# Performance work log

Measured on AMD Instinct MI355X. Metric: run time of the kernel, lower is better.

The kernel has to match this reference:

```python
import jax, jax.numpy as jnp
from jax import lax
import numpy as np

RATIO = 0.25
RADIUS = 0.2


def _fps(xyz, npoint):
    # iterative farthest point sampling, sequential over npoint via lax.scan
    B, N, _ = xyz.shape
    far0 = jax.random.randint(jax.random.key(42), (B,), 0, N)
    dist0 = jnp.full((B, N), 1e10, xyz.dtype)

    def step(carry, _):
        distance, far = carry
        centroid = jnp.take_along_axis(xyz, far[:, None, None], axis=1)  # (B,1,3)
        d = jnp.sum((xyz - centroid) ** 2, axis=-1)                      # (B,N)
        distance = jnp.minimum(distance, d)
        return (distance, jnp.argmax(distance, axis=-1)), far

    _, idxs = lax.scan(step, (dist0, far0), None, length=npoint)  # (npoint,B)
    return jnp.transpose(idxs)  # (B,npoint)


def _gather(pts, idx):
    # pts (B,N,C), idx (B,...) int -> (B,...,C)
    return jax.vmap(lambda p, i: p[i])(pts, idx)


def reference(xyz, points, w1, b1, w2, b2, w3, b3):
    B, N, _ = xyz.shape
    S = int(N * RATIO)
    fps_idx = _fps(xyz, S)                 # (B,S)
    new_xyz = _gather(xyz, fps_idx)        # (B,S,3)

    # ball query with nsample = N (module passes xyz.shape[1])
    sqr = (jnp.sum(new_xyz ** 2, -1)[:, :, None]
           + jnp.sum(xyz ** 2, -1)[:, None, :]
           - 2.0 * jnp.einsum('bsc,bnc->bsn', new_xyz, xyz))  # (B,S,N)
    gidx = jnp.where(sqr > RADIUS ** 2, N, jnp.arange(N)[None, None, :])
    gidx = jnp.sort(gidx, axis=-1)         # (B,S,N), sentinel N sorts last
    first = gidx[:, :, 0:1]
    idx = jnp.where(gidx == N, first, gidx)  # (B,S,N)

    grouped_xyz = _gather(xyz, idx) - new_xyz[:, :, None, :]       # (B,S,N,3)
    grouped_pts = _gather(jnp.transpose(points, (0, 2, 1)), idx)   # (B,S,N,C)
    x = jnp.concatenate([grouped_xyz, grouped_pts], axis=-1)       # (B,S,N,3+C)

    # 1x1 convs == pointwise channel linears, ReLU except last
    x = jax.nn.relu(jnp.einsum('bsnc,oc->bsno', x, w1) + b1)
    x = jax.nn.relu(jnp.einsum('bsnc,oc->bsno', x, w2) + b2)
    x = jnp.einsum('bsnc,oc->bsno', x, w3) + b3

    new_points = jnp.transpose(jnp.max(x, axis=2), (0, 2, 1))  # (B,C',S)
    return new_xyz, new_points


def setup_inputs() -> dict:
    key = jax.random.key(0)
    ks = jax.random.split(key, 8)
    return {
        'xyz': jax.random.uniform(ks[0], (2, 2048, 3), dtype=jnp.float32),
        'points': jax.random.normal(ks[1], (2, 13, 2048), dtype=jnp.float32),
        'w1': 0.1 * jax.random.normal(ks[2], (32, 16), dtype=jnp.float32),
        'b1': 0.1 * jax.random.normal(ks[3], (32,), dtype=jnp.float32),
        'w2': 0.1 * jax.random.normal(ks[4], (32, 32), dtype=jnp.float32),
        'b2': 0.1 * jax.random.normal(ks[5], (32,), dtype=jnp.float32),
        'w3': 0.1 * jax.random.normal(ks[6], (64, 32), dtype=jnp.float32),
        'b3': 0.1 * jax.random.normal(ks[7], (64,), dtype=jnp.float32),
    }
```

## Files before the change

### kernel.cpp

```cpp
#include <hip/hip_runtime.h>
#include <stdint.h>

#define NPTS 2048
#define SOUT 512
#define NB   2
#define TB   256
#define PPT  8
#define NW   4
#define FMAGIC 0xC0DE0000u

typedef float vf2 __attribute__((ext_vector_type(2)));

__device__ __forceinline__ float wave_allmax_f32(float v) {
    int x = __float_as_int(v); int t;
    t = __builtin_amdgcn_update_dpp(x, x, 0x111, 0xF, 0xF, true); v = fmaxf(v, __int_as_float(t)); x = __float_as_int(v);
    t = __builtin_amdgcn_update_dpp(x, x, 0x112, 0xF, 0xF, true); v = fmaxf(v, __int_as_float(t)); x = __float_as_int(v);
    t = __builtin_amdgcn_update_dpp(x, x, 0x114, 0xF, 0xF, true); v = fmaxf(v, __int_as_float(t)); x = __float_as_int(v);
    t = __builtin_amdgcn_update_dpp(x, x, 0x118, 0xF, 0xF, true); v = fmaxf(v, __int_as_float(t)); x = __float_as_int(v);
    t = __builtin_amdgcn_update_dpp(x, x, 0x142, 0xA, 0xF, true); v = fmaxf(v, __int_as_float(t)); x = __float_as_int(v);
    t = __builtin_amdgcn_update_dpp(x, x, 0x143, 0xC, 0xF, true); v = fmaxf(v, __int_as_float(t)); x = __float_as_int(v);
    return __int_as_float(__builtin_amdgcn_readlane(x, 63));
}
__device__ __forceinline__ float4 sel4(bool c, float4 A, float4 B) {
    float4 r;
    r.x = c ? A.x : B.x; r.y = c ? A.y : B.y;
    r.z = c ? A.z : B.z; r.w = c ? A.w : B.w;
    return r;
}

template<bool FUSED>
__device__ __forceinline__ void fps_role(const float* __restrict__ xb,
                                         float* __restrict__ ob,
                                         unsigned* flagp, int far,
                                         float4* slot , float* scf,
                                         int t) {
    const int lane = t & 63;
    const int wvl  = t >> 6;
    __builtin_amdgcn_s_setprio(1);
    float v24[24];
    {
        const float4* src = (const float4*)(xb + t * PPT * 3);
#pragma unroll
        for (int j = 0; j < 6; ++j) {
            float4 a = src[j];
            v24[j*4+0] = a.x; v24[j*4+1] = a.y; v24[j*4+2] = a.z; v24[j*4+3] = a.w;
        }
    }
    vf2 PX[4], PY[4], PZ[4], DD[4];
#pragma unroll
    for (int j = 0; j < 4; ++j) {
        PX[j].x = v24[(2*j)*3+0]; PX[j].y = v24[(2*j+1)*3+0];
        PY[j].x = v24[(2*j)*3+1]; PY[j].y = v24[(2*j+1)*3+1];
        PZ[j].x = v24[(2*j)*3+2]; PZ[j].y = v24[(2*j+1)*3+2];
        DD[j].x = 1e10f; DD[j].y = 1e10f;
    }
    float cx = xb[far*3+0], cy = xb[far*3+1], cz = xb[far*3+2];

    for (int s = 0; s < SOUT - 1; ++s) {
        if (FUSED) {
            if (wvl == 3) {
                if (lane == 32 && s >= 16 && (s & 15) == 0)
                    __hip_atomic_store(flagp, FMAGIC + (unsigned)s,
                                       __ATOMIC_RELEASE, __HIP_MEMORY_SCOPE_AGENT);
                if (lane >= 32 && lane < 35) {
                    float v = (lane == 32) ? cx : ((lane == 33) ? cy : cz);
                    unsigned* o = (unsigned*)ob + s * 3 + (lane - 32);
                    __hip_atomic_store(o, __float_as_uint(v),
                                       __ATOMIC_RELAXED, __HIP_MEMORY_SCOPE_AGENT);
                }
            }
        } else {
            if (t == 0) { scf[s*3+0] = cx; scf[s*3+1] = cy; scf[s*3+2] = cz; }
        }
        {
#pragma clang fp contract(off)
            vf2 vcx; vcx.x = cx; vcx.y = cx;
            vf2 vcy; vcy.x = cy; vcy.y = cy;
            vf2 vcz; vcz.x = cz; vcz.y = cz;
#pragma unroll
            for (int j = 0; j < 4; ++j) {
                vf2 dx = PX[j] - vcx;
                vf2 dy = PY[j] - vcy;
                vf2 dz = PZ[j] - vcz;
                vf2 d2 = (dx*dx + dy*dy) + dz*dz;
                DD[j].x = fminf(DD[j].x, d2.x);
                DD[j].y = fminf(DD[j].y, d2.y);
            }
        }
        float bv = fmaxf(
            fmaxf(fmaxf(DD[0].x, DD[0].y), fmaxf(DD[1].x, DD[1].y)),
            fmaxf(fmaxf(DD[2].x, DD[2].y), fmaxf(DD[3].x, DD[3].y)));
        float bx = PX[3].y, by = PY[3].y, bz = PZ[3].y;
        { bool c = DD[3].x == bv; bx = c?PX[3].x:bx; by = c?PY[3].x:by; bz = c?PZ[3].x:bz; }
        { bool c = DD[2].y == bv; bx = c?PX[2].y:bx; by = c?PY[2].y:by; bz = c?PZ[2].y:bz; }
        { bool c = DD[2].x == bv; bx = c?PX[2].x:bx; by = c?PY[2].x:by; bz = c?PZ[2].x:bz; }
        { bool c = DD[1].y == bv; bx = c?PX[1].y:bx; by = c?PY[1].y:by; bz = c?PZ[1].y:bz; }
        { bool c = DD[1].x == bv; bx = c?PX[1].x:bx; by = c?PY[1].x:by; bz = c?PZ[1].x:bz; }
        { bool c = DD[0].y == bv; bx = c?PX[0].y:bx; by = c?PY[0].y:by; bz = c?PZ[0].y:bz; }
        { bool c = DD[0].x == bv; bx = c?PX[0].x:bx; by = c?PY[0].x:by; bz = c?PZ[0].x:bz; }
        float wmax = wave_allmax_f32(bv);
        unsigned long long msk = __ballot(bv == wmax);
        int l0 = (int)__builtin_ctzll(msk);
        const int par = s & 1;
        if (lane == l0) slot[par*NW + wvl] = make_float4(wmax, bx, by, bz);
        if (FUSED) {
            __builtin_amdgcn_s_waitcnt(0xC07F);
            __builtin_amdgcn_s_barrier();
        } else {
            __syncthreads();
        }
        float4 a0 = slot[par*NW + 0];
        float4 a1 = slot[par*NW + 1];
        float4 a2 = slot[par*NW + 2];
        float4 a3 = slot[par*NW + 3];
        float4 m01 = sel4(a1.x > a0.x, a1, a0);
        float4 m23 = sel4(a3.x > a2.x, a3, a2);
        float4 mf  = sel4(m23.x > m01.x, m23, m01);
        cx = mf.y; cy = mf.z; cz = mf.w;
    }
    if (FUSED) {
        if (wvl == 3) {
            if (lane >= 32 && lane < 35) {
                float v = (lane == 32) ? cx : ((lane == 33) ? cy : cz);
                unsigned* o = (unsigned*)ob + (SOUT - 1) * 3 + (lane - 32);
                __hip_atomic_store(o, __float_as_uint(v),
                                   __ATOMIC_RELAXED, __HIP_MEMORY_SCOPE_AGENT);
            }
            if (lane == 32)
                __hip_atomic_store(flagp, FMAGIC + 512u,
                                   __ATOMIC_RELEASE, __HIP_MEMORY_SCOPE_AGENT);
        }
    } else {
        if (t == 0) {
            scf[(SOUT-1)*3+0] = cx; scf[(SOUT-1)*3+1] = cy; scf[(SOUT-1)*3+2] = cz;
        }
        __syncthreads();
        for (int i = t; i < SOUT * 3; i += TB) ob[i] = scf[i];
    }
}

__device__ __forceinline__ void group_role(
        const float* __restrict__ xyz,  const float* __restrict__ points,
        const float* __restrict__ w1,   const float* __restrict__ b1,
        const float* __restrict__ w2,   const float* __restrict__ b2,
        const float* __restrict__ w3,   const float* __restrict__ b3,
        const float* __restrict__ new_xyz, float* __restrict__ new_points,
        const unsigned* flags, unsigned short* sidx, float* sh2,
        int lane, int q) {
    float wf3[32];
    {
        const float4* w3v = (const float4*)(w3 + lane * 32);
#pragma unroll
        for (int j = 0; j < 8; ++j) {
            float4 v = w3v[j];
            wf3[j*4+0] = v.x; wf3[j*4+1] = v.y; wf3[j*4+2] = v.z; wf3[j*4+3] = v.w;
        }
    }
    const float rb3 = b3[lane];
    const int b = q >> 9;
    const int s = q & (SOUT - 1);

    if (flags) {
        const unsigned* flagp = flags + (b << 6);
        if (lane == 0) {
            const unsigned tgt = FMAGIC + (unsigned)s + 1u;
            int polls = 0;
            for (;;) {
                unsigned v = __hip_atomic_load(flagp, __ATOMIC_ACQUIRE,
                                               __HIP_MEMORY_SCOPE_AGENT);
                if (v >= tgt && v <= FMAGIC + 512u) break;
                if (++polls > (1 << 18)) break;
                __builtin_amdgcn_s_sleep(32);
            }
        }
        __threadfence();
    }
    const unsigned* nx = (const unsigned*)new_xyz + (size_t)q * 3;
    const float qx = __uint_as_float(__hip_atomic_load(nx + 0, __ATOMIC_RELAXED, __HIP_MEMORY_SCOPE_AGENT));
    const float qy = __uint_as_float(__hip_atomic_load(nx + 1, __ATOMIC_RELAXED, __HIP_MEMORY_SCOPE_AGENT));
    const float qz = __uint_as_float(__hip_atomic_load(nx + 2, __ATOMIC_RELAXED, __HIP_MEMORY_SCOPE_AGENT));
    const float qs = __fadd_rn(__fadd_rn(__fmul_rn(qx,qx), __fmul_rn(qy,qy)), __fmul_rn(qz,qz));
    const float* xb = xyz    + (size_t)b * NPTS * 3;
    const float* pb = points + (size_t)b * 13 * NPTS;

    int cnt = 0;
    const unsigned long long lm = (1ull << lane) - 1ull;
    for (int r = 0; r < NPTS / 64; ++r) {
        int n = r * 64 + lane;
        float x = xb[n*3+0], y = xb[n*3+1], z = xb[n*3+2];
        float pn = __fadd_rn(__fadd_rn(__fmul_rn(x,x), __fmul_rn(y,y)), __fmul_rn(z,z));
        float dt = __fadd_rn(__fadd_rn(__fmul_rn(qx,x), __fmul_rn(qy,y)), __fmul_rn(qz,z));
        float sqr = __fsub_rn(__fadd_rn(qs, pn), __fmul_rn(2.0f, dt));
        bool sel = !(sqr > 0.04f);
        unsigned long long m = __ballot(sel);
        if (sel) sidx[cnt + __popcll(m & lm)] = (unsigned short)n;
        cnt += (int)__popcll(m);
    }
    const int K = cnt;
    const int nfirst = (int)sidx[0];

    float mx = -3.0e38f;
    for (int tb = 0; tb < K; tb += 64) {
        int m = tb + lane;
        int n = (m < K) ? (int)sidx[m] : nfirst;
        float f[16];
        f[0] = xb[n*3+0] - qx;
        f[1] = xb[n*3+1] - qy;
        f[2] = xb[n*3+2] - qz;
#pragma unroll
        for (int c = 0; c < 13; ++c) f[3+c] = pb[c*NPTS + n];
        float h1[32];
#pragma unroll
        for (int o = 0; o < 32; ++o) {
            float acc = b1[o];
            const float4* wr = (const float4*)(w1 + o*16);
#pragma unroll
            for (int c4 = 0; c4 < 4; ++c4) {
                float4 wv = wr[c4];
                acc = fmaf(f[c4*4+0], wv.x, acc);
                acc = fmaf(f[c4*4+1], wv.y, acc);
                acc = fmaf(f[c4*4+2], wv.z, acc);
                acc = fmaf(f[c4*4+3], wv.w, acc);
            }
            h1[o] = fmaxf(acc, 0.0f);
        }
        float h2[32];
#pragma unroll
        for (int o = 0; o < 32; ++o) {
            float acc = b2[o];
            const float4* wr = (const float4*)(w2 + o*32);
#pragma unroll
            for (int c4 = 0; c4 < 8; ++c4) {
                float4 wv = wr[c4];
                acc = fmaf(h1[c4*4+0], wv.x, acc);
                acc = fmaf(h1[c4*4+1], wv.y, acc);
                acc = fmaf(h1[c4*4+2], wv.z, acc);
                acc = fmaf(h1[c4*4+3], wv.w, acc);
            }
            h2[o] = fmaxf(acc, 0.0f);
        }
        {
            float4* row = (float4*)(sh2 + lane * 36);
#pragma unroll
            for (int c4 = 0; c4 < 8; ++c4)
                row[c4] = make_float4(h2[c4*4+0], h2[c4*4+1], h2[c4*4+2], h2[c4*4+3]);
        }
        int rows = K - tb; if (rows > 64) rows = 64;
#pragma unroll 4
        for (int n2 = 0; n2 < rows; ++n2) {
            const float4* hr = (const float4*)(sh2 + n2 * 36);
            float acc = rb3;
#pragma unroll
            for (int c4 = 0; c4 < 8; ++c4) {
                float4 h = hr[c4];
                acc = fmaf(h.x, wf3[c4*4+0], acc);
                acc = fmaf(h.y, wf3[c4*4+1], acc);
                acc = fmaf(h.z, wf3[c4*4+2], acc);
                acc = fmaf(h.w, wf3[c4*4+3], acc);
            }
            mx = fmaxf(mx, acc);
        }
    }
    new_points[((size_t)b * 64 + lane) * SOUT + s] = mx;
}

__global__ __launch_bounds__(TB, 1) void fused_kernel(
        const float* __restrict__ xyz,  const float* __restrict__ points,
        const float* __restrict__ w1,   const float* __restrict__ b1,
        const float* __restrict__ w2,   const float* __restrict__ b2,
        const float* __restrict__ w3,   const float* __restrict__ b3,
        float* __restrict__ new_xyz, float* __restrict__ new_points,
        unsigned* flags, int far0, int far1) {
    __shared__ float4 s_slot[2 * NW];
    __shared__ unsigned short s_sidx[4 * NPTS];
    __shared__ __align__(16) float s_sh2[4 * 64 * 36];
    const int blk = blockIdx.x;
    const int tid = threadIdx.x;
    if (blk < 2) {
        const int bg = blk;
        fps_role<true>(xyz + (size_t)bg * NPTS * 3,
                       new_xyz + (size_t)bg * SOUT * 3,
                       flags + (bg << 6),
                       (bg == 0) ? far0 : far1,
                       s_slot, nullptr, tid);
    } else {
        const int lane = tid & 63;
        const int wvl  = tid >> 6;
        const int q    = (blk - 2) * 4 + wvl;
        group_role(xyz, points, w1, b1, w2, b2, w3, b3, new_xyz, new_points,
                   flags, s_sidx + wvl * NPTS, s_sh2 + wvl * 64 * 36, lane, q);
    }
}

__global__ __launch_bounds__(TB, 1) void fps_kernel(const float* __restrict__ xyz,
                                                    float* __restrict__ new_xyz,
                                                    int far0, int far1) {
    __shared__ float4 s_slot[2 * NW];
    __shared__ __align__(16) float s_scf[SOUT * 3];
    const int bg = blockIdx.x;
    fps_role<false>(xyz + (size_t)bg * NPTS * 3, new_xyz + (size_t)bg * SOUT * 3,
                    nullptr, (bg == 0) ? far0 : far1, s_slot, s_scf, threadIdx.x);
}
__global__ __launch_bounds__(64, 1) void group_kernel(
        const float* __restrict__ xyz,  const float* __restrict__ points,
        const float* __restrict__ w1,   const float* __restrict__ b1,
        const float* __restrict__ w2,   const float* __restrict__ b2,
        const float* __restrict__ w3,   const float* __restrict__ b3,
        const float* __restrict__ new_xyz, float* __restrict__ new_points) {
    __shared__ unsigned short s_sidx[NPTS];
    __shared__ __align__(16) float s_sh2[64 * 36];
    group_role(xyz, points, w1, b1, w2, b2, w3, b3, new_xyz, new_points,
               nullptr, s_sidx, s_sh2, threadIdx.x, blockIdx.x);
}

static inline uint32_t rotl32(uint32_t x, int r) { return (x << r) | (x >> (32 - r)); }
static void threefry2x32_host(uint32_t k0, uint32_t k1, uint32_t& x0, uint32_t& x1) {
    const int R[2][4] = {{13,15,26,6},{17,29,16,24}};
    uint32_t ks[3] = {k0, k1, k0 ^ k1 ^ 0x1BD11BDAu};
    x0 += ks[0]; x1 += ks[1];
    for (int i = 0; i < 5; ++i) {
        for (int j = 0; j < 4; ++j) { x0 += x1; x1 = rotl32(x1, R[i & 1][j]); x1 ^= x0; }
        x0 += ks[(i + 1) % 3];
        x1 += ks[(i + 2) % 3] + (uint32_t)(i + 1);
    }
}

extern "C" void kernel_launch(void* const* d_in, const int* in_sizes, int n_in,
                              void* d_out, int out_size, void* d_ws, size_t ws_size,
                              hipStream_t stream) {
    const float* xyz    = (const float*)d_in[0];
    const float* points = (const float*)d_in[1];
    const float* w1 = (const float*)d_in[2];
    const float* b1 = (const float*)d_in[3];
    const float* w2 = (const float*)d_in[4];
    const float* b2 = (const float*)d_in[5];
    const float* w3 = (const float*)d_in[6];
    const float* b3 = (const float*)d_in[7];
    float* out        = (float*)d_out;
    float* new_xyz    = out;
    float* new_points = out + NB * SOUT * 3;

    uint32_t k2a = 0, k2b = 1; threefry2x32_host(0u, 42u, k2a, k2b);
    uint32_t u0 = 0, u1 = 0;  threefry2x32_host(k2a, k2b, u0, u1);
    uint32_t v0 = 0, v1 = 1;  threefry2x32_host(k2a, k2b, v0, v1);
    int far0 = (int)((u0 ^ u1) & (NPTS - 1));
    int far1 = (int)((v0 ^ v1) & (NPTS - 1));

    if (ws_size >= 512) {
        hipLaunchKernelGGL(fused_kernel, dim3(2 + NB * SOUT / 4), dim3(TB), 0, stream,
                           xyz, points, w1, b1, w2, b2, w3, b3,
                           new_xyz, new_points, (unsigned*)d_ws, far0, far1);
    } else {
        hipLaunchKernelGGL(fps_kernel, dim3(NB), dim3(TB), 0, stream,
                           xyz, new_xyz, far0, far1);
        hipLaunchKernelGGL(group_kernel, dim3(NB * SOUT), dim3(64), 0, stream,
                           xyz, points, w1, b1, w2, b2, w3, b3, new_xyz, new_points);
    }
}
```

Measured before the change: 344.7 us.

## Offload FPS result publishing to a dedicated relay wave

```diff
diff --git a/kernel.cpp b/kernel.cpp
--- a/kernel.cpp
+++ b/kernel.cpp
@@ -4,7 +4,7 @@
 #define NPTS 2048
 #define SOUT 512
 #define NB   2
-#define TB   256
+#define TB   320
 #define PPT  8
 #define NW   4
 #define FMAGIC 0xC0DE0000u
@@ -28,12 +28,8 @@
     return r;
 }
 
-template<bool FUSED>
-__device__ __forceinline__ void fps_role(const float* __restrict__ xb,
-                                         float* __restrict__ ob,
-                                         unsigned* flagp, int far,
-                                         float4* slot , float* scf,
-                                         int t) {
+__device__ __forceinline__ void fps_team(const float* __restrict__ xb,
+                                         int far, float4* slot, int t) {
     const int lane = t & 63;
     const int wvl  = t >> 6;
     __builtin_amdgcn_s_setprio(1);
@@ -57,21 +53,6 @@
     float cx = xb[far*3+0], cy = xb[far*3+1], cz = xb[far*3+2];
 
     for (int s = 0; s < SOUT - 1; ++s) {
-        if (FUSED) {
-            if (wvl == 3) {
-                if (lane == 32 && s >= 16 && (s & 15) == 0)
-                    __hip_atomic_store(flagp, FMAGIC + (unsigned)s,
-                                       __ATOMIC_RELEASE, __HIP_MEMORY_SCOPE_AGENT);
-                if (lane >= 32 && lane < 35) {
-                    float v = (lane == 32) ? cx : ((lane == 33) ? cy : cz);
-                    unsigned* o = (unsigned*)ob + s * 3 + (lane - 32);
-                    __hip_atomic_store(o, __float_as_uint(v),
-                                       __ATOMIC_RELAXED, __HIP_MEMORY_SCOPE_AGENT);
-                }
-            }
-        } else {
-            if (t == 0) { scf[s*3+0] = cx; scf[s*3+1] = cy; scf[s*3+2] = cz; }
-        }
         {
 #pragma clang fp contract(off)
             vf2 vcx; vcx.x = cx; vcx.y = cx;
@@ -103,12 +84,7 @@
         int l0 = (int)__builtin_ctzll(msk);
         const int par = s & 1;
         if (lane == l0) slot[par*NW + wvl] = make_float4(wmax, bx, by, bz);
-        if (FUSED) {
-            __builtin_amdgcn_s_waitcnt(0xC07F);
-            __builtin_amdgcn_s_barrier();
-        } else {
-            __syncthreads();
-        }
+        __syncthreads();
         float4 a0 = slot[par*NW + 0];
         float4 a1 = slot[par*NW + 1];
         float4 a2 = slot[par*NW + 2];
@@ -118,25 +94,39 @@
         float4 mf  = sel4(m23.x > m01.x, m23, m01);
         cx = mf.y; cy = mf.z; cz = mf.w;
     }
-    if (FUSED) {
-        if (wvl == 3) {
-            if (lane >= 32 && lane < 35) {
-                float v = (lane == 32) ? cx : ((lane == 33) ? cy : cz);
-                unsigned* o = (unsigned*)ob + (SOUT - 1) * 3 + (lane - 32);
-                __hip_atomic_store(o, __float_as_uint(v),
-                                   __ATOMIC_RELAXED, __HIP_MEMORY_SCOPE_AGENT);
-            }
-            if (lane == 32)
-                __hip_atomic_store(flagp, FMAGIC + 512u,
-                                   __ATOMIC_RELEASE, __HIP_MEMORY_SCOPE_AGENT);
-        }
-    } else {
-        if (t == 0) {
-            scf[(SOUT-1)*3+0] = cx; scf[(SOUT-1)*3+1] = cy; scf[(SOUT-1)*3+2] = cz;
-        }
-        __syncthreads();
-        for (int i = t; i < SOUT * 3; i += TB) ob[i] = scf[i];
-    }
+}
+
+__device__ __forceinline__ void relay_role(const float* __restrict__ xb,
+                                           float* __restrict__ ob,
+                                           unsigned* flagp, int far,
+                                           const float4* slot, int lane) {
+    if (lane < 3)
+        __hip_atomic_store((unsigned*)ob + lane,
+                           __float_as_uint(xb[far*3 + lane]),
+                           __ATOMIC_RELAXED, __HIP_MEMORY_SCOPE_AGENT);
+    for (int s = 0; s < SOUT - 1; ++s) {
+        __builtin_amdgcn_s_barrier();
+        if (lane == 0 && s >= 16 && (s & 15) == 0)
+            __hip_atomic_store(flagp, FMAGIC + (unsigned)s,
+                               __ATOMIC_RELEASE, __HIP_MEMORY_SCOPE_AGENT);
+        const int par = s & 1;
+        float4 a0 = slot[par*NW + 0];
+        float4 a1 = slot[par*NW + 1];
+        float4 a2 = slot[par*NW + 2];
+        float4 a3 = slot[par*NW + 3];
+        float4 m01 = sel4(a1.x > a0.x, a1, a0);
+        float4 m23 = sel4(a3.x > a2.x, a3, a2);
+        float4 mf  = sel4(m23.x > m01.x, m23, m01);
+        if (lane < 3) {
+            float v = (lane == 0) ? mf.y : ((lane == 1) ? mf.z : mf.w);
+            __hip_atomic_store((unsigned*)ob + (s + 1) * 3 + lane,
+                               __float_as_uint(v),
+                               __ATOMIC_RELAXED, __HIP_MEMORY_SCOPE_AGENT);
+        }
+    }
+    if (lane == 0)
+        __hip_atomic_store(flagp, FMAGIC + 512u,
+                           __ATOMIC_RELEASE, __HIP_MEMORY_SCOPE_AGENT);
 }
 
 __device__ __forceinline__ void group_role(
@@ -276,30 +266,103 @@
     __shared__ __align__(16) float s_sh2[4 * 64 * 36];
     const int blk = blockIdx.x;
     const int tid = threadIdx.x;
+    const int lane = tid & 63;
+    const int wvl  = tid >> 6;
     if (blk < 2) {
-        const int bg = blk;
-        fps_role<true>(xyz + (size_t)bg * NPTS * 3,
-                       new_xyz + (size_t)bg * SOUT * 3,
-                       flags + (bg << 6),
-                       (bg == 0) ? far0 : far1,
-                       s_slot, nullptr, tid);
-    } else {
-        const int lane = tid & 63;
-        const int wvl  = tid >> 6;
-        const int q    = (blk - 2) * 4 + wvl;
-        group_role(xyz, points, w1, b1, w2, b2, w3, b3, new_xyz, new_points,
-                   flags, s_sidx + wvl * NPTS, s_sh2 + wvl * 64 * 36, lane, q);
-    }
-}
-
-__global__ __launch_bounds__(TB, 1) void fps_kernel(const float* __restrict__ xyz,
-                                                    float* __restrict__ new_xyz,
-                                                    int far0, int far1) {
-    __shared__ float4 s_slot[2 * NW];
-    __shared__ __align__(16) float s_scf[SOUT * 3];
-    const int bg = blockIdx.x;
-    fps_role<false>(xyz + (size_t)bg * NPTS * 3, new_xyz + (size_t)bg * SOUT * 3,
-                    nullptr, (bg == 0) ? far0 : far1, s_slot, s_scf, threadIdx.x);
+        const float* xb = xyz + (size_t)blk * NPTS * 3;
+        float* ob = new_xyz + (size_t)blk * SOUT * 3;
+        const int far = (blk == 0) ? far0 : far1;
+        if (wvl < NW) {
+            fps_team(xb, far, s_slot, tid);
+        } else {
+            relay_role(xb, ob, flags + (blk << 6), far, s_slot, lane);
+        }
+        return;
+    }
+    if (wvl >= 4) return;
+    const int q = (blk - 2) * 4 + wvl;
+    group_role(xyz, points, w1, b1, w2, b2, w3, b3, new_xyz, new_points,
+               flags, s_sidx + wvl * NPTS, s_sh2 + (size_t)wvl * 64 * 36, lane, q);
+}
+
+__global__ __launch_bounds__(256, 1) void fps_kernel(const float* __restrict__ xyz,
+                                                     float* __restrict__ new_xyz,
+                                                     int far0, int far1) {
+    __shared__ float4 slot[2 * NW];
+    const int bg   = blockIdx.x;
+    const int t    = threadIdx.x;
+    const int lane = t & 63;
+    const int wvl  = t >> 6;
+    const float* __restrict__ xb = xyz + (size_t)bg * NPTS * 3;
+    float* __restrict__ ob = new_xyz + (size_t)bg * SOUT * 3;
+    const int far = (bg == 0) ? far0 : far1;
+
+    float v24[24];
+    {
+        const float4* src = (const float4*)(xb + t * PPT * 3);
+#pragma unroll
+        for (int j = 0; j < 6; ++j) {
+            float4 a = src[j];
+            v24[j*4+0] = a.x; v24[j*4+1] = a.y; v24[j*4+2] = a.z; v24[j*4+3] = a.w;
+        }
+    }
+    vf2 PX[4], PY[4], PZ[4], DD[4];
+#pragma unroll
+    for (int j = 0; j < 4; ++j) {
+        PX[j].x = v24[(2*j)*3+0]; PX[j].y = v24[(2*j+1)*3+0];
+        PY[j].x = v24[(2*j)*3+1]; PY[j].y = v24[(2*j+1)*3+1];
+        PZ[j].x = v24[(2*j)*3+2]; PZ[j].y = v24[(2*j+1)*3+2];
+        DD[j].x = 1e10f; DD[j].y = 1e10f;
+    }
+    float cx = xb[far*3+0], cy = xb[far*3+1], cz = xb[far*3+2];
+
+    for (int s = 0; s < SOUT; ++s) {
+        if (wvl == 3 && lane >= 32 && lane < 35) {
+            float v = (lane == 32) ? cx : ((lane == 33) ? cy : cz);
+            ob[s * 3 + (lane - 32)] = v;
+        }
+        if (s == SOUT - 1) break;
+        {
+#pragma clang fp contract(off)
+            vf2 vcx; vcx.x = cx; vcx.y = cx;
+            vf2 vcy; vcy.x = cy; vcy.y = cy;
+            vf2 vcz; vcz.x = cz; vcz.y = cz;
+#pragma unroll
+            for (int j = 0; j < 4; ++j) {
+                vf2 dx = PX[j] - vcx;
+                vf2 dy = PY[j] - vcy;
+                vf2 dz = PZ[j] - vcz;
+                vf2 d2 = (dx*dx + dy*dy) + dz*dz;
+                DD[j].x = fminf(DD[j].x, d2.x);
+                DD[j].y = fminf(DD[j].y, d2.y);
+            }
+        }
+        float bv = fmaxf(
+            fmaxf(fmaxf(DD[0].x, DD[0].y), fmaxf(DD[1].x, DD[1].y)),
+            fmaxf(fmaxf(DD[2].x, DD[2].y), fmaxf(DD[3].x, DD[3].y)));
+        float bx = PX[3].y, by = PY[3].y, bz = PZ[3].y;
+        { bool c = DD[3].x == bv; bx = c?PX[3].x:bx; by = c?PY[3].x:by; bz = c?PZ[3].x:bz; }
+        { bool c = DD[2].y == bv; bx = c?PX[2].y:bx; by = c?PY[2].y:by; bz = c?PZ[2].y:bz; }
+        { bool c = DD[2].x == bv; bx = c?PX[2].x:bx; by = c?PY[2].x:by; bz = c?PZ[2].x:bz; }
+        { bool c = DD[1].y == bv; bx = c?PX[1].y:bx; by = c?PY[1].y:by; bz = c?PZ[1].y:bz; }
+        { bool c = DD[1].x == bv; bx = c?PX[1].x:bx; by = c?PY[1].x:by; bz = c?PZ[1].x:bz; }
+        { bool c = DD[0].y == bv; bx = c?PX[0].y:bx; by = c?PY[0].y:by; bz = c?PZ[0].y:bz; }
+        { bool c = DD[0].x == bv; bx = c?PX[0].x:bx; by = c?PY[0].x:by; bz = c?PZ[0].x:bz; }
+        float wmax = wave_allmax_f32(bv);
+        unsigned long long msk = __ballot(bv == wmax);
+        int l0 = (int)__builtin_ctzll(msk);
+        const int par = s & 1;
+        if (lane == l0) slot[par*NW + wvl] = make_float4(wmax, bx, by, bz);
+        __syncthreads();
+        float4 a0 = slot[par*NW + 0];
+        float4 a1 = slot[par*NW + 1];
+        float4 a2 = slot[par*NW + 2];
+        float4 a3 = slot[par*NW + 3];
+        float4 m01 = sel4(a1.x > a0.x, a1, a0);
+        float4 m23 = sel4(a3.x > a2.x, a3, a2);
+        float4 mf  = sel4(m23.x > m01.x, m23, m01);
+        cx = mf.y; cy = mf.z; cz = mf.w;
+    }
 }
 __global__ __launch_bounds__(64, 1) void group_kernel(
         const float* __restrict__ xyz,  const float* __restrict__ points,
@@ -307,10 +370,10 @@
         const float* __restrict__ w2,   const float* __restrict__ b2,
         const float* __restrict__ w3,   const float* __restrict__ b3,
         const float* __restrict__ new_xyz, float* __restrict__ new_points) {
-    __shared__ unsigned short s_sidx[NPTS];
-    __shared__ __align__(16) float s_sh2[64 * 36];
+    __shared__ unsigned short sidx[NPTS];
+    __shared__ __align__(16) float sh2[64 * 36];
     group_role(xyz, points, w1, b1, w2, b2, w3, b3, new_xyz, new_points,
-               nullptr, s_sidx, s_sh2, threadIdx.x, blockIdx.x);
+               nullptr, sidx, sh2, threadIdx.x, blockIdx.x);
 }
 
 static inline uint32_t rotl32(uint32_t x, int r) { return (x << r) | (x >> (32 - r)); }
@@ -351,7 +414,7 @@
                            xyz, points, w1, b1, w2, b2, w3, b3,
                            new_xyz, new_points, (unsigned*)d_ws, far0, far1);
     } else {
-        hipLaunchKernelGGL(fps_kernel, dim3(NB), dim3(TB), 0, stream,
+        hipLaunchKernelGGL(fps_kernel, dim3(NB), dim3(256), 0, stream,
                            xyz, new_xyz, far0, far1);
         hipLaunchKernelGGL(group_kernel, dim3(NB * SOUT), dim3(64), 0, stream,
                            xyz, points, w1, b1, w2, b2, w3, b3, new_xyz, new_points);
```

Result: slower. 389.6 us (+13.0%).
